# Performance work log

Hardware: AMD Instinct MI355X
Metric: run time of the kernel (lower is better)

Reference implementation:

```python
import jax, jax.numpy as jnp
import numpy as np

B, T, C = 4, 4096, 1024
ATT_SCALE = 1.0
TIME_MIX_RATIO = 1.0


def setup_inputs() -> dict:
    key = jax.random.key(0)
    ks = jax.random.split(key, 7)
    std = 0.02  # 0.02 * (layer_id + 1), layer_id = 0
    x = jax.random.normal(ks[0], (B, T, C), dtype=jnp.float32)
    state = jnp.zeros((B, C), dtype=jnp.float32)
    W_r = jax.random.normal(ks[1], (C, C), dtype=jnp.float32) * std
    W_k = jax.random.normal(ks[2], (C, C), dtype=jnp.float32) * std
    W_v = jax.random.normal(ks[3], (C, C), dtype=jnp.float32) * std
    W_o = jax.random.normal(ks[4], (C, C), dtype=jnp.float32) * std
    time_mix_r = jnp.ones((1, 1, C), dtype=jnp.float32) * TIME_MIX_RATIO
    time_mix_k = jnp.ones((1, 1, C), dtype=jnp.float32) * TIME_MIX_RATIO
    time_mix_v = jnp.ones((1, 1, C), dtype=jnp.float32) * TIME_MIX_RATIO
    # learned log-decay; use negative values so exp(time_decay) < 1 and the
    # recurrence is numerically stable over T=4096 steps (a trained model
    # would have such values; the torch init 0.9 would blow up for long T)
    time_decay = jax.random.uniform(ks[5], (C,), dtype=jnp.float32,
                                    minval=-0.1, maxval=-0.01)
    return {"x": x, "state": state, "W_r": W_r, "W_k": W_k, "W_v": W_v,
            "W_o": W_o, "time_mix_r": time_mix_r, "time_mix_k": time_mix_k,
            "time_mix_v": time_mix_v, "time_decay": time_decay}


def reference(x, state, W_r, W_k, W_v, W_o,
              time_mix_r, time_mix_k, time_mix_v, time_decay):
    # shifted input: previous-token stream, seeded with incoming state
    x_mix = jnp.concatenate([state[:, None, :], x[:, :-1]], axis=1)  # [B,T,C]

    r_in = x * time_mix_r + x_mix * (1.0 - time_mix_r)
    k_in = x * time_mix_k + x_mix * (1.0 - time_mix_k)
    v_in = x * time_mix_v + x_mix * (1.0 - time_mix_v)

    r = jax.nn.sigmoid(jnp.einsum('btc,dc->btd', r_in, W_r))
    k = jnp.exp(jnp.einsum('btc,dc->btd', k_in, W_k))
    v = jnp.einsum('btc,dc->btd', v_in, W_v)

    decay = jnp.exp(time_decay)  # [C]
    kv = k * v                   # [B,T,C]

    def step(s, inp):
        kv_t, r_t = inp          # each [B,C]
        s = s * decay + kv_t
        return s, r_t * s

    _, out = jax.lax.scan(step, state,
                          (kv.transpose(1, 0, 2), r.transpose(1, 0, 2)))
    out = out.transpose(1, 0, 2) * ATT_SCALE          # [B,T,C]

    output = jnp.einsum('btc,dc->btd', out, W_o)      # time_output
    new_state = x[:, -1]
    return output, new_state
```

## Files before the change

kernel.cpp:

```cpp
#include <hip/hip_runtime.h>

#define B_ 4
#define T_ 4096
#define C_ 1024
#define M_ (B_*T_)
#define BTC (B_*T_*C_)
#define NCHUNK 64
#define CHUNK (T_ / NCHUNK)

typedef unsigned short u16;
typedef __attribute__((ext_vector_type(8))) short bf16x8;
typedef __attribute__((ext_vector_type(8))) unsigned short u16x8;
typedef __attribute__((ext_vector_type(4))) float f32x4;

static __device__ __forceinline__ u16 f2bf(float f) {
    unsigned u = __float_as_uint(f);
    unsigned r = (u + 0x7FFFu + ((u >> 16) & 1u)) >> 16;
    return (u16)r;
}
static __device__ __forceinline__ float bf2f(u16 h) {
    return __uint_as_float(((unsigned)h) << 16);
}

__global__ void prep_kernel(const float* __restrict__ x, const float* __restrict__ state,
                            const float* __restrict__ tmr, const float* __restrict__ tmk,
                            const float* __restrict__ tmv,
                            u16* __restrict__ rin, u16* __restrict__ kin, u16* __restrict__ vin,
                            float* __restrict__ new_state) {
    const int idx = blockIdx.x * 256 + threadIdx.x;
    const int c8 = idx & 127;
    const int bt = idx >> 7;
    const int t  = bt & (T_ - 1);
    const int b  = bt >> 12;

    const float4* xv = (const float4*)x;
    float4 xa = xv[idx * 2], xb = xv[idx * 2 + 1];
    float4 pa, pb;
    if (t == 0) {
        const float4* sv = (const float4*)state;
        pa = sv[(b * 128 + c8) * 2]; pb = sv[(b * 128 + c8) * 2 + 1];
    } else {
        pa = xv[(idx - 128) * 2]; pb = xv[(idx - 128) * 2 + 1];
    }
    float4 mra = ((const float4*)tmr)[c8 * 2], mrb = ((const float4*)tmr)[c8 * 2 + 1];
    float4 mka = ((const float4*)tmk)[c8 * 2], mkb = ((const float4*)tmk)[c8 * 2 + 1];
    float4 mva = ((const float4*)tmv)[c8 * 2], mvb = ((const float4*)tmv)[c8 * 2 + 1];

    float xc[8] = {xa.x, xa.y, xa.z, xa.w, xb.x, xb.y, xb.z, xb.w};
    float xp[8] = {pa.x, pa.y, pa.z, pa.w, pb.x, pb.y, pb.z, pb.w};
    float mr[8] = {mra.x, mra.y, mra.z, mra.w, mrb.x, mrb.y, mrb.z, mrb.w};
    float mk[8] = {mka.x, mka.y, mka.z, mka.w, mkb.x, mkb.y, mkb.z, mkb.w};
    float mv[8] = {mva.x, mva.y, mva.z, mva.w, mvb.x, mvb.y, mvb.z, mvb.w};

    u16x8 pr, pk, pv;
#pragma unroll
    for (int j = 0; j < 8; ++j) {
        pr[j] = f2bf(xc[j] * mr[j] + xp[j] * (1.f - mr[j]));
        pk[j] = f2bf(xc[j] * mk[j] + xp[j] * (1.f - mk[j]));
        pv[j] = f2bf(xc[j] * mv[j] + xp[j] * (1.f - mv[j]));
    }
    ((u16x8*)rin)[idx] = pr;
    ((u16x8*)kin)[idx] = pk;
    ((u16x8*)vin)[idx] = pv;
    if (t == T_ - 1) {
        ((float4*)new_state)[(b * 128 + c8) * 2]     = xa;
        ((float4*)new_state)[(b * 128 + c8) * 2 + 1] = xb;
    }
}

__global__ void cast_all_kernel(const float* __restrict__ w0, const float* __restrict__ w1,
                                const float* __restrict__ w2, const float* __restrict__ w3,
                                u16* __restrict__ dst) {
    int w = blockIdx.x >> 10;
    int i = ((blockIdx.x & 1023) << 8) + threadIdx.x;
    const float* src = (w == 0) ? w0 : (w == 1) ? w1 : (w == 2) ? w2 : w3;
    float4 v = ((const float4*)src)[i];
    ushort4 o;
    o.x = f2bf(v.x); o.y = f2bf(v.y); o.z = f2bf(v.z); o.w = f2bf(v.w);
    ((ushort4*)(dst + (size_t)w * C_ * C_))[i] = o;
}

#define EPI_SIG  0
#define EPI_EXP  1
#define EPI_BF16 2
#define EPI_F32  3

template <int EPI>
__global__ __launch_bounds__(512, 2)
void gemm256(const u16* __restrict__ A, const u16* __restrict__ W, void* __restrict__ Cptr) {
    extern __shared__ __align__(16) u16 smem[];
    u16* sA = smem;
    u16* sB = smem + 3 * 16384;

    const int N = C_, K = C_;
    const int nk = K / 64;

    const int tid  = threadIdx.x;
    const int wid  = tid >> 6, lane = tid & 63;
    const int wr   = wid >> 2, wc = wid & 3;
    const int lr   = lane & 15, kq = lane >> 4;

    const int wg   = blockIdx.x;
    const int wgid = (wg & 7) * 32 + (wg >> 3);
    const int bm   = wgid >> 2, bn = wgid & 3;
    const int row0 = bm * 256, col0 = bn * 256;

    f32x4 acc[8][4];
#pragma unroll
    for (int i = 0; i < 8; ++i)
#pragma unroll
        for (int j = 0; j < 4; ++j)
#pragma unroll
            for (int q = 0; q < 4; ++q) acc[i][j][q] = 0.f;

    const int rl = tid >> 3;
    const int uu = tid & 7;
    const int usw = uu ^ (rl & 7);

    auto stA = [&](int buf, int h, int kt) {
#pragma unroll
        for (int p = 0; p < 2; ++p) {
            int rt = h * 128 + p * 64 + rl;
            const u16* g = A + (size_t)(row0 + rt) * K + kt * 64 + usw * 8;
            __builtin_amdgcn_global_load_lds(
                (const __attribute__((address_space(1))) void*)g,
                (__attribute__((address_space(3))) void*)&sA[buf * 16384 + rt * 64 + uu * 8],
                16, 0, 0);
        }
    };
    auto stB = [&](int buf, int h, int kt) {
#pragma unroll
        for (int p = 0; p < 2; ++p) {
            int rt = h * 128 + p * 64 + rl;
            const u16* g = W + (size_t)(col0 + rt) * K + kt * 64 + usw * 8;
            __builtin_amdgcn_global_load_lds(
                (const __attribute__((address_space(1))) void*)g,
                (__attribute__((address_space(3))) void*)&sB[buf * 16384 + rt * 64 + uu * 8],
                16, 0, 0);
        }
    };
    auto ldA = [&](int buf, int ig, int ks) -> bf16x8 {
        int R = wr * 128 + ig * 16 + lr;
        int unit = (ks * 4 + kq) ^ (lr & 7);
        return *(const bf16x8*)&sA[buf * 16384 + R * 64 + unit * 8];
    };
    auto ldB = [&](int buf, int j, int ks) -> bf16x8 {
        int R = wc * 64 + j * 16 + lr;
        int unit = (ks * 4 + kq) ^ (lr & 7);
        return *(const bf16x8*)&sB[buf * 16384 + R * 64 + unit * 8];
    };

    stA(0, 0, 0); stA(0, 1, 0); stB(0, 0, 0); stB(0, 1, 0);
    stA(1, 0, 1); stA(1, 1, 1); stB(1, 0, 1); stB(1, 1, 1);
    asm volatile("s_waitcnt vmcnt(8)" ::: "memory");
    __builtin_amdgcn_s_barrier();

    for (int kt = 0; kt < nk; ++kt) {
        const int curA = kt % 3, curB = kt & 1;
        const int dstA = (kt + 2) % 3;
        const int t2   = (kt + 2 < nk) ? kt + 2 : nk - 1;

        bf16x8 b[4][2];
        {
            bf16x8 a[2][2];
#pragma unroll
            for (int j = 0; j < 4; ++j)
#pragma unroll
                for (int ks = 0; ks < 2; ++ks) b[j][ks] = ldB(curB, j, ks);
#pragma unroll
            for (int i = 0; i < 2; ++i)
#pragma unroll
                for (int ks = 0; ks < 2; ++ks) a[i][ks] = ldA(curA, i, ks);
            stA(dstA, 0, t2);
            __builtin_amdgcn_s_barrier();
            asm volatile("s_waitcnt lgkmcnt(0)" ::: "memory");
            __builtin_amdgcn_sched_barrier(0);
            __builtin_amdgcn_s_setprio(1);
#pragma unroll
            for (int i = 0; i < 2; ++i)
#pragma unroll
                for (int j = 0; j < 4; ++j)
#pragma unroll
                    for (int ks = 0; ks < 2; ++ks)
                        acc[i][j] = __builtin_amdgcn_mfma_f32_16x16x32_bf16(b[j][ks], a[i][ks], acc[i][j], 0, 0, 0);
            __builtin_amdgcn_s_setprio(0);
            __builtin_amdgcn_s_barrier();
        }
        {
            bf16x8 a[2][2];
#pragma unroll
            for (int i = 0; i < 2; ++i)
#pragma unroll
                for (int ks = 0; ks < 2; ++ks) a[i][ks] = ldA(curA, 2 + i, ks);
            stA(dstA, 1, t2);
            __builtin_amdgcn_s_barrier();
            asm volatile("s_waitcnt lgkmcnt(0)" ::: "memory");
            __builtin_amdgcn_sched_barrier(0);
            __builtin_amdgcn_s_setprio(1);
#pragma unroll
            for (int i = 0; i < 2; ++i)
#pragma unroll
                for (int j = 0; j < 4; ++j)
#pragma unroll
                    for (int ks = 0; ks < 2; ++ks)
                        acc[2 + i][j] = __builtin_amdgcn_mfma_f32_16x16x32_bf16(b[j][ks], a[i][ks], acc[2 + i][j], 0, 0, 0);
            __builtin_amdgcn_s_setprio(0);
            __builtin_amdgcn_s_barrier();
        }
        {
            bf16x8 a[2][2];
#pragma unroll
            for (int i = 0; i < 2; ++i)
#pragma unroll
                for (int ks = 0; ks < 2; ++ks) a[i][ks] = ldA(curA, 4 + i, ks);
            stB(curB, 0, t2);
            __builtin_amdgcn_s_barrier();
            asm volatile("s_waitcnt lgkmcnt(0)" ::: "memory");
            __builtin_amdgcn_sched_barrier(0);
            __builtin_amdgcn_s_setprio(1);
#pragma unroll
            for (int i = 0; i < 2; ++i)
#pragma unroll
                for (int j = 0; j < 4; ++j)
#pragma unroll
                    for (int ks = 0; ks < 2; ++ks)
                        acc[4 + i][j] = __builtin_amdgcn_mfma_f32_16x16x32_bf16(b[j][ks], a[i][ks], acc[4 + i][j], 0, 0, 0);
            __builtin_amdgcn_s_setprio(0);
            __builtin_amdgcn_s_barrier();
        }
        {
            bf16x8 a[2][2];
#pragma unroll
            for (int i = 0; i < 2; ++i)
#pragma unroll
                for (int ks = 0; ks < 2; ++ks) a[i][ks] = ldA(curA, 6 + i, ks);
            stB(curB, 1, t2);
            __builtin_amdgcn_s_barrier();
            asm volatile("s_waitcnt lgkmcnt(0)" ::: "memory");
            __builtin_amdgcn_sched_barrier(0);
            __builtin_amdgcn_s_setprio(1);
#pragma unroll
            for (int i = 0; i < 2; ++i)
#pragma unroll
                for (int j = 0; j < 4; ++j)
#pragma unroll
                    for (int ks = 0; ks < 2; ++ks)
                        acc[6 + i][j] = __builtin_amdgcn_mfma_f32_16x16x32_bf16(b[j][ks], a[i][ks], acc[6 + i][j], 0, 0, 0);
            __builtin_amdgcn_s_setprio(0);
            asm volatile("s_waitcnt vmcnt(8)" ::: "memory");
            __builtin_amdgcn_s_barrier();
        }
    }

    const int r0 = row0 + wr * 128;
    const int c0 = col0 + wc * 64;
#pragma unroll
    for (int i = 0; i < 8; ++i) {
        const int rr = r0 + i * 16 + lr;
#pragma unroll
        for (int j = 0; j < 4; ++j) {
            const int cc = c0 + j * 16 + kq * 4;
            f32x4 v = acc[i][j];
            if constexpr (EPI == EPI_F32) {
                float4 o = {v[0], v[1], v[2], v[3]};
                *(float4*)((float*)Cptr + (size_t)rr * N + cc) = o;
            } else {
                ushort4 o;
                if constexpr (EPI == EPI_SIG) {
                    o.x = f2bf(1.0f / (1.0f + __expf(-v[0])));
                    o.y = f2bf(1.0f / (1.0f + __expf(-v[1])));
                    o.z = f2bf(1.0f / (1.0f + __expf(-v[2])));
                    o.w = f2bf(1.0f / (1.0f + __expf(-v[3])));
                } else if constexpr (EPI == EPI_EXP) {
                    o.x = f2bf(__expf(v[0])); o.y = f2bf(__expf(v[1]));
                    o.z = f2bf(__expf(v[2])); o.w = f2bf(__expf(v[3]));
                } else {
                    o.x = f2bf(v[0]); o.y = f2bf(v[1]);
                    o.z = f2bf(v[2]); o.w = f2bf(v[3]);
                }
                *(ushort4*)((u16*)Cptr + (size_t)rr * N + cc) = o;
            }
        }
    }
}

__global__ void scan_partial(const u16* __restrict__ ek, const u16* __restrict__ vv,
                             const float* __restrict__ td, float* __restrict__ S) {
    const int tid = threadIdx.x;
    const int bid = blockIdx.x;
    const int ct  = bid & 3;
    const int j   = (bid >> 2) & (NCHUNK - 1);
    const int b   = bid >> 8;
    const int c   = ct * 256 + tid;
    const float d = __expf(td[c]);
    float s = 0.f;
    size_t base = ((size_t)(b * T_ + j * CHUNK)) * C_ + c;
#pragma unroll 4
    for (int t = 0; t < CHUNK; ++t) {
        size_t ix = base + (size_t)t * C_;
        s = s * d + bf2f(ek[ix]) * bf2f(vv[ix]);
    }
    S[((size_t)(b * NCHUNK + j)) * C_ + c] = s;
}

__global__ void scan_carry(const float* __restrict__ S, const float* __restrict__ td,
                           const float* __restrict__ state, float* __restrict__ carry) {
    int id = blockIdx.x * blockDim.x + threadIdx.x;
    if (id >= B_ * C_) return;
    int c = id & (C_ - 1);
    int b = id >> 10;
    float dl = __expf(td[c] * (float)CHUNK);
    float E = state[id];
#pragma unroll 8
    for (int j = 0; j < NCHUNK; ++j) {
        size_t o = ((size_t)(b * NCHUNK + j)) * C_ + c;
        carry[o] = E;
        E = dl * E + S[o];
    }
}

__global__ void scan_apply(const u16* __restrict__ ek, const u16* __restrict__ vv,
                           const u16* __restrict__ rr, const float* __restrict__ td,
                           const float* __restrict__ carry, u16* __restrict__ out) {
    const int tid = threadIdx.x;
    const int bid = blockIdx.x;
    const int ct  = bid & 3;
    const int j   = (bid >> 2) & (NCHUNK - 1);
    const int b   = bid >> 8;
    const int c   = ct * 256 + tid;
    const float d = __expf(td[c]);
    float s = carry[((size_t)(b * NCHUNK + j)) * C_ + c];
    size_t base = ((size_t)(b * T_ + j * CHUNK)) * C_ + c;
#pragma unroll 4
    for (int t = 0; t < CHUNK; ++t) {
        size_t ix = base + (size_t)t * C_;
        s = s * d + bf2f(ek[ix]) * bf2f(vv[ix]);
        out[ix] = f2bf(s * bf2f(rr[ix]));
    }
}

extern "C" void kernel_launch(void* const* d_in, const int* in_sizes, int n_in,
                              void* d_out, int out_size, void* d_ws, size_t ws_size,
                              hipStream_t stream) {
    const float* x     = (const float*)d_in[0];
    const float* state = (const float*)d_in[1];
    const float* W_r   = (const float*)d_in[2];
    const float* W_k   = (const float*)d_in[3];
    const float* W_v   = (const float*)d_in[4];
    const float* W_o   = (const float*)d_in[5];
    const float* tmr   = (const float*)d_in[6];
    const float* tmk   = (const float*)d_in[7];
    const float* tmv   = (const float*)d_in[8];
    const float* td    = (const float*)d_in[9];

    float* out_f     = (float*)d_out;
    float* new_state = out_f + (size_t)BTC;

    char* ws = (char*)d_ws;
    const size_t SZ = (size_t)BTC * 2;
    u16* rin   = (u16*)(ws + 0 * SZ);
    u16* kin   = (u16*)(ws + 1 * SZ);
    u16* vin   = (u16*)(ws + 2 * SZ);
    u16* rbuf  = (u16*)(ws + 3 * SZ);
    u16* ekbuf = (u16*)(ws + 4 * SZ);
    u16* vbuf  = (u16*)(ws + 5 * SZ);
    u16* wts   = (u16*)(ws + 6 * SZ);
    u16* wrb   = wts;
    u16* wkb   = wrb + (size_t)C_ * C_;
    u16* wvb   = wkb + (size_t)C_ * C_;
    u16* wob   = wvb + (size_t)C_ * C_;
    float* Sbuf  = (float*)(wob + (size_t)C_ * C_);
    float* cbuf  = Sbuf + (size_t)B_ * NCHUNK * C_;
    u16* outb  = vin;

    const int LDSB = 5 * 16384 * 2;
    (void)hipFuncSetAttribute((const void*)gemm256<EPI_SIG>,  hipFuncAttributeMaxDynamicSharedMemorySize, LDSB);
    (void)hipFuncSetAttribute((const void*)gemm256<EPI_EXP>,  hipFuncAttributeMaxDynamicSharedMemorySize, LDSB);
    (void)hipFuncSetAttribute((const void*)gemm256<EPI_BF16>, hipFuncAttributeMaxDynamicSharedMemorySize, LDSB);
    (void)hipFuncSetAttribute((const void*)gemm256<EPI_F32>,  hipFuncAttributeMaxDynamicSharedMemorySize, LDSB);

    prep_kernel<<<BTC / 8 / 256, 256, 0, stream>>>(
        x, state, tmr, tmk, tmv, rin, kin, vin, new_state);

    cast_all_kernel<<<4096, 256, 0, stream>>>(W_r, W_k, W_v, W_o, wts);

    gemm256<EPI_SIG ><<<256, 512, LDSB, stream>>>(rin, wrb, (void*)rbuf);
    gemm256<EPI_EXP ><<<256, 512, LDSB, stream>>>(kin, wkb, (void*)ekbuf);
    gemm256<EPI_BF16><<<256, 512, LDSB, stream>>>(vin, wvb, (void*)vbuf);

    const int nscan_blocks = B_ * NCHUNK * (C_ / 256);
    scan_partial<<<nscan_blocks, 256, 0, stream>>>(ekbuf, vbuf, td, Sbuf);
    scan_carry<<<(B_ * C_ + 255) / 256, 256, 0, stream>>>(Sbuf, td, state, cbuf);
    scan_apply<<<nscan_blocks, 256, 0, stream>>>(ekbuf, vbuf, rbuf, td, cbuf, outb);

    gemm256<EPI_F32><<<256, 512, LDSB, stream>>>(outb, wob, (void*)out_f);
}
```

Baseline: 250.9 us.

## Fuse prep with weight cast, interleave r/k/v inputs, and fold k*v into v GEMM

Merges the weight-cast kernel into the prep kernel so one launch handles both, and writes r/k/v mixed inputs into a single interleaved buffer with row pitch 3C that the GEMMs read through a new stride argument. The v-projection GEMM epilogue now multiplies by the exp(k) result, so the scans read a single kv buffer instead of separate ek and v streams. This cuts one launch and one bf16 read stream from each scan pass. In exchange, the v GEMM epilogue gains an extra read of ek, and kv is rounded to bf16 once after the product.

```diff
diff --git a/kernel.cpp b/kernel.cpp
--- a/kernel.cpp
+++ b/kernel.cpp
@@ -22,12 +22,26 @@
     return __uint_as_float(((unsigned)h) << 16);
 }
 
-__global__ void prep_kernel(const float* __restrict__ x, const float* __restrict__ state,
-                            const float* __restrict__ tmr, const float* __restrict__ tmk,
-                            const float* __restrict__ tmv,
-                            u16* __restrict__ rin, u16* __restrict__ kin, u16* __restrict__ vin,
-                            float* __restrict__ new_state) {
-    const int idx = blockIdx.x * 256 + threadIdx.x;
+__global__ void prep_cast_kernel(const float* __restrict__ x, const float* __restrict__ state,
+                                 const float* __restrict__ tmr, const float* __restrict__ tmk,
+                                 const float* __restrict__ tmv,
+                                 const float* __restrict__ w0, const float* __restrict__ w1,
+                                 const float* __restrict__ w2, const float* __restrict__ w3,
+                                 u16* __restrict__ rkv, u16* __restrict__ wts,
+                                 float* __restrict__ new_state) {
+    const int bid = blockIdx.x;
+    if (bid >= 4096) {
+        int i = (bid - 4096) * 512 + threadIdx.x;
+        int w = i >> 18;
+        int j = i & 262143;
+        const float* src = (w == 0) ? w0 : (w == 1) ? w1 : (w == 2) ? w2 : w3;
+        float4 v = ((const float4*)src)[j];
+        ushort4 o;
+        o.x = f2bf(v.x); o.y = f2bf(v.y); o.z = f2bf(v.z); o.w = f2bf(v.w);
+        ((ushort4*)(wts + (size_t)w * C_ * C_))[j] = o;
+        return;
+    }
+    const int idx = bid * 512 + threadIdx.x;
     const int c8 = idx & 127;
     const int bt = idx >> 7;
     const int t  = bt & (T_ - 1);
@@ -59,35 +73,25 @@
         pk[j] = f2bf(xc[j] * mk[j] + xp[j] * (1.f - mk[j]));
         pv[j] = f2bf(xc[j] * mv[j] + xp[j] * (1.f - mv[j]));
     }
-    ((u16x8*)rin)[idx] = pr;
-    ((u16x8*)kin)[idx] = pk;
-    ((u16x8*)vin)[idx] = pv;
+    u16x8* dst = (u16x8*)rkv + (size_t)bt * 384 + c8;
+    dst[0]   = pr;
+    dst[128] = pk;
+    dst[256] = pv;
     if (t == T_ - 1) {
         ((float4*)new_state)[(b * 128 + c8) * 2]     = xa;
         ((float4*)new_state)[(b * 128 + c8) * 2 + 1] = xb;
     }
 }
 
-__global__ void cast_all_kernel(const float* __restrict__ w0, const float* __restrict__ w1,
-                                const float* __restrict__ w2, const float* __restrict__ w3,
-                                u16* __restrict__ dst) {
-    int w = blockIdx.x >> 10;
-    int i = ((blockIdx.x & 1023) << 8) + threadIdx.x;
-    const float* src = (w == 0) ? w0 : (w == 1) ? w1 : (w == 2) ? w2 : w3;
-    float4 v = ((const float4*)src)[i];
-    ushort4 o;
-    o.x = f2bf(v.x); o.y = f2bf(v.y); o.z = f2bf(v.z); o.w = f2bf(v.w);
-    ((ushort4*)(dst + (size_t)w * C_ * C_))[i] = o;
-}
-
 #define EPI_SIG  0
 #define EPI_EXP  1
-#define EPI_BF16 2
+#define EPI_KV   2
 #define EPI_F32  3
 
 template <int EPI>
 __global__ __launch_bounds__(512, 2)
-void gemm256(const u16* __restrict__ A, const u16* __restrict__ W, void* __restrict__ Cptr) {
+void gemm256(const u16* __restrict__ A, int ap, const u16* __restrict__ W,
+             const u16* __restrict__ EK, void* __restrict__ Cptr) {
     extern __shared__ __align__(16) u16 smem[];
     u16* sA = smem;
     u16* sB = smem + 3 * 16384;
@@ -121,7 +125,7 @@
 #pragma unroll
         for (int p = 0; p < 2; ++p) {
             int rt = h * 128 + p * 64 + rl;
-            const u16* g = A + (size_t)(row0 + rt) * K + kt * 64 + usw * 8;
+            const u16* g = A + (size_t)(row0 + rt) * ap + kt * 64 + usw * 8;
             __builtin_amdgcn_global_load_lds(
                 (const __attribute__((address_space(1))) void*)g,
                 (__attribute__((address_space(3))) void*)&sA[buf * 16384 + rt * 64 + uu * 8],
@@ -275,8 +279,11 @@
                     o.x = f2bf(__expf(v[0])); o.y = f2bf(__expf(v[1]));
                     o.z = f2bf(__expf(v[2])); o.w = f2bf(__expf(v[3]));
                 } else {
-                    o.x = f2bf(v[0]); o.y = f2bf(v[1]);
-                    o.z = f2bf(v[2]); o.w = f2bf(v[3]);
+                    ushort4 ek = *(const ushort4*)(EK + (size_t)rr * N + cc);
+                    o.x = f2bf(bf2f(ek.x) * v[0]);
+                    o.y = f2bf(bf2f(ek.y) * v[1]);
+                    o.z = f2bf(bf2f(ek.z) * v[2]);
+                    o.w = f2bf(bf2f(ek.w) * v[3]);
                 }
                 *(ushort4*)((u16*)Cptr + (size_t)rr * N + cc) = o;
             }
@@ -284,8 +291,8 @@
     }
 }
 
-__global__ void scan_partial(const u16* __restrict__ ek, const u16* __restrict__ vv,
-                             const float* __restrict__ td, float* __restrict__ S) {
+__global__ void scan_partial(const u16* __restrict__ kv, const float* __restrict__ td,
+                             float* __restrict__ S) {
     const int tid = threadIdx.x;
     const int bid = blockIdx.x;
     const int ct  = bid & 3;
@@ -297,8 +304,7 @@
     size_t base = ((size_t)(b * T_ + j * CHUNK)) * C_ + c;
 #pragma unroll 4
     for (int t = 0; t < CHUNK; ++t) {
-        size_t ix = base + (size_t)t * C_;
-        s = s * d + bf2f(ek[ix]) * bf2f(vv[ix]);
+        s = s * d + bf2f(kv[base + (size_t)t * C_]);
     }
     S[((size_t)(b * NCHUNK + j)) * C_ + c] = s;
 }
@@ -319,9 +325,9 @@
     }
 }
 
-__global__ void scan_apply(const u16* __restrict__ ek, const u16* __restrict__ vv,
-                           const u16* __restrict__ rr, const float* __restrict__ td,
-                           const float* __restrict__ carry, u16* __restrict__ out) {
+__global__ void scan_apply(const u16* __restrict__ kv, const u16* __restrict__ rr,
+                           const float* __restrict__ td, const float* __restrict__ carry,
+                           u16* __restrict__ out) {
     const int tid = threadIdx.x;
     const int bid = blockIdx.x;
     const int ct  = bid & 3;
@@ -334,7 +340,7 @@
 #pragma unroll 4
     for (int t = 0; t < CHUNK; ++t) {
         size_t ix = base + (size_t)t * C_;
-        s = s * d + bf2f(ek[ix]) * bf2f(vv[ix]);
+        s = s * d + bf2f(kv[ix]);
         out[ix] = f2bf(s * bf2f(rr[ix]));
     }
 }
@@ -358,12 +364,10 @@
 
     char* ws = (char*)d_ws;
     const size_t SZ = (size_t)BTC * 2;
-    u16* rin   = (u16*)(ws + 0 * SZ);
-    u16* kin   = (u16*)(ws + 1 * SZ);
-    u16* vin   = (u16*)(ws + 2 * SZ);
+    u16* rkv   = (u16*)(ws + 0 * SZ);
     u16* rbuf  = (u16*)(ws + 3 * SZ);
     u16* ekbuf = (u16*)(ws + 4 * SZ);
-    u16* vbuf  = (u16*)(ws + 5 * SZ);
+    u16* kvbuf = (u16*)(ws + 5 * SZ);
     u16* wts   = (u16*)(ws + 6 * SZ);
     u16* wrb   = wts;
     u16* wkb   = wrb + (size_t)C_ * C_;
@@ -371,27 +375,25 @@
     u16* wob   = wvb + (size_t)C_ * C_;
     float* Sbuf  = (float*)(wob + (size_t)C_ * C_);
     float* cbuf  = Sbuf + (size_t)B_ * NCHUNK * C_;
-    u16* outb  = vin;
+    u16* outb  = ekbuf;
 
     const int LDSB = 5 * 16384 * 2;
-    (void)hipFuncSetAttribute((const void*)gemm256<EPI_SIG>,  hipFuncAttributeMaxDynamicSharedMemorySize, LDSB);
-    (void)hipFuncSetAttribute((const void*)gemm256<EPI_EXP>,  hipFuncAttributeMaxDynamicSharedMemorySize, LDSB);
-    (void)hipFuncSetAttribute((const void*)gemm256<EPI_BF16>, hipFuncAttributeMaxDynamicSharedMemorySize, LDSB);
-    (void)hipFuncSetAttribute((const void*)gemm256<EPI_F32>,  hipFuncAttributeMaxDynamicSharedMemorySize, LDSB);
-
-    prep_kernel<<<BTC / 8 / 256, 256, 0, stream>>>(
-        x, state, tmr, tmk, tmv, rin, kin, vin, new_state);
-
-    cast_all_kernel<<<4096, 256, 0, stream>>>(W_r, W_k, W_v, W_o, wts);
-
-    gemm256<EPI_SIG ><<<256, 512, LDSB, stream>>>(rin, wrb, (void*)rbuf);
-    gemm256<EPI_EXP ><<<256, 512, LDSB, stream>>>(kin, wkb, (void*)ekbuf);
-    gemm256<EPI_BF16><<<256, 512, LDSB, stream>>>(vin, wvb, (void*)vbuf);
+    (void)hipFuncSetAttribute((const void*)gemm256<EPI_SIG>, hipFuncAttributeMaxDynamicSharedMemorySize, LDSB);
+    (void)hipFuncSetAttribute((const void*)gemm256<EPI_EXP>, hipFuncAttributeMaxDynamicSharedMemorySize, LDSB);
+    (void)hipFuncSetAttribute((const void*)gemm256<EPI_KV>,  hipFuncAttributeMaxDynamicSharedMemorySize, LDSB);
+    (void)hipFuncSetAttribute((const void*)gemm256<EPI_F32>, hipFuncAttributeMaxDynamicSharedMemorySize, LDSB);
+
+    prep_cast_kernel<<<4096 + 2048, 512, 0, stream>>>(
+        x, state, tmr, tmk, tmv, W_r, W_k, W_v, W_o, rkv, wts, new_state);
+
+    gemm256<EPI_SIG><<<256, 512, LDSB, stream>>>(rkv,          3 * C_, wrb, nullptr, (void*)rbuf);
+    gemm256<EPI_EXP><<<256, 512, LDSB, stream>>>(rkv + C_,     3 * C_, wkb, nullptr, (void*)ekbuf);
+    gemm256<EPI_KV ><<<256, 512, LDSB, stream>>>(rkv + 2 * C_, 3 * C_, wvb, ekbuf,   (void*)kvbuf);
 
     const int nscan_blocks = B_ * NCHUNK * (C_ / 256);
-    scan_partial<<<nscan_blocks, 256, 0, stream>>>(ekbuf, vbuf, td, Sbuf);
+    scan_partial<<<nscan_blocks, 256, 0, stream>>>(kvbuf, td, Sbuf);
     scan_carry<<<(B_ * C_ + 255) / 256, 256, 0, stream>>>(Sbuf, td, state, cbuf);
-    scan_apply<<<nscan_blocks, 256, 0, stream>>>(ekbuf, vbuf, rbuf, td, cbuf, outb);
-
-    gemm256<EPI_F32><<<256, 512, LDSB, stream>>>(outb, wob, (void*)out_f);
-}
+    scan_apply<<<nscan_blocks, 256, 0, stream>>>(kvbuf, rbuf, td, cbuf, outb);
+
+    gemm256<EPI_F32><<<256, 512, LDSB, stream>>>(outb, C_, wob, nullptr, (void*)out_f);
+}
```

Result: faster. 243.1 us (-3.1%).
